# Kernel optimization log

Hardware: AMD Instinct MI355X
Metric: run time of the kernel (lower is better)

## Reference

```python
import jax, jax.numpy as jnp
import numpy as np

N_NODES = 20000
N_EDGES = 320000
IN_DIM = 256
OUT_DIM = 256
NUM_RELS = 8
NUM_BASES = 4


def setup_inputs() -> dict:
    key = jax.random.key(0)
    k = jax.random.split(key, 7)
    return {
        "h": jax.random.normal(k[0], (N_NODES, IN_DIM), dtype=jnp.float32),
        "basis": jax.random.normal(k[1], (NUM_BASES, IN_DIM, OUT_DIM), dtype=jnp.float32)
        * (6.0 / (IN_DIM + OUT_DIM)) ** 0.5,
        "w_comp": jax.random.normal(k[2], (NUM_RELS, NUM_BASES), dtype=jnp.float32),
        "bias": jax.random.normal(k[3], (OUT_DIM,), dtype=jnp.float32) * 0.01,
        "src": jax.random.randint(k[4], (N_EDGES,), 0, N_NODES, dtype=jnp.int32),
        "dst": jax.random.randint(k[5], (N_EDGES,), 0, N_NODES, dtype=jnp.int32),
        "etype": jax.random.randint(k[6], (N_EDGES,), 0, NUM_RELS, dtype=jnp.int32),
    }


def reference(h, basis, w_comp, bias, src, dst, etype):
    # Faithful to the torch basis-decomposition quirk:
    #   weight.view(in, B, out); matmul(w_comp, .) -> [in, R, out]; view -> [R, in, out]
    in_dim, out_dim = h.shape[1], basis.shape[2]
    num_rels = w_comp.shape[0]
    wr = basis.reshape(in_dim, NUM_BASES, out_dim)          # raw-buffer reinterpret (torch .view)
    weight = jnp.einsum("rb,ibo->iro", w_comp, wr)          # [in, R, out]
    weight = weight.reshape(num_rels, in_dim, out_dim)      # raw-buffer reinterpret (torch .view)

    # msg_e = h[src_e] @ weight[etype_e]. Group by relation: transform all nodes
    # under every relation weight (dense GEMMs), then gather per edge.
    t = jnp.einsum("nd,rdo->rno", h, weight)                # [R, N, out]
    msg = t[etype, src]                                     # [E, out]

    # scatter-sum aggregation to destination nodes (dgl fn.sum)
    agg = jax.ops.segment_sum(msg, dst, num_segments=h.shape[0])  # [N, out]
    return jax.nn.relu(agg + bias)
```

## Files before the change

kernel.cpp:

```cpp
#include <hip/hip_runtime.h>


#define N_NODES  20000
#define N_EDGES  320000
#define IN_DIM   256
#define OUT_DIM  256
#define NUM_RELS 8
#define KDIM     128
#define M_PAD    20032
#define CAP      96

#define FOLD_BLOCKS 2500
#define FILL_BLOCKS 1250
#define BP_BLOCKS   128

typedef __attribute__((ext_vector_type(8)))  short short8;
typedef __attribute__((ext_vector_type(16))) float float16v;

static __device__ __forceinline__ unsigned f2bf_rne(float x) {
    unsigned u = __float_as_uint(x);
    return (u + 0x7fffu + ((u >> 16) & 1u)) >> 16;
}
static __device__ __forceinline__ float bf2f(unsigned b) {
    return __uint_as_float(b << 16);
}

__global__ __launch_bounds__(256)
void prep_kernel(const float* __restrict__ h, const float* __restrict__ w_comp,
                 unsigned short* __restrict__ U,
                 const int* __restrict__ src, const int* __restrict__ dst,
                 const int* __restrict__ et,
                 int* __restrict__ cnt, int* __restrict__ bucket,
                 const float* __restrict__ basis, unsigned short* __restrict__ Bp) {
    int b = blockIdx.x;
    int t = threadIdx.x;
    if (b < FOLD_BLOCKS) {
        int gid = b * 256 + t;
        int n = gid >> 5, k = gid & 31;
        const float* hp = h + (size_t)n * IN_DIM + k * 8;
        float4 h0 = *(const float4*)hp;
        float4 h1 = *(const float4*)(hp + 4);
        float hv[8] = {h0.x, h0.y, h0.z, h0.w, h1.x, h1.y, h1.z, h1.w};
        float a0 = 0.f, a1 = 0.f, a2 = 0.f, a3 = 0.f;
#pragma unroll
        for (int j = 0; j < 8; ++j) {
            float hj = hv[j];
            a0 += hj * w_comp[j * 4 + 0];
            a1 += hj * w_comp[j * 4 + 1];
            a2 += hj * w_comp[j * 4 + 2];
            a3 += hj * w_comp[j * 4 + 3];
        }
        uint2 p;
        p.x = f2bf_rne(a0) | (f2bf_rne(a1) << 16);
        p.y = f2bf_rne(a2) | (f2bf_rne(a3) << 16);
        *(uint2*)(U + ((size_t)n << 7) + k * 4) = p;
    } else if (b < FOLD_BLOCKS + FILL_BLOCKS) {
        int e = (b - FOLD_BLOCKS) * 256 + t;
        int d = dst[e];
        int p = atomicAdd(&cnt[d], 1);
        if (p < CAP) bucket[(size_t)d * CAP + p] = src[e] | (et[e] << 16);
    } else {
        int frag = (b - FOLD_BLOCKS - FILL_BLOCKS) * 256 + t;
        int lane = frag & 63;
        int ks   = (frag >> 6) & 7;
        int r    = (frag >> 9) & 7;
        int ct   = frag >> 12;
        int o  = ct * 32 + (lane & 31);
        int kb = r * 128 + ks * 16 + (lane >> 5) * 8;
        const float* bsp = basis + (size_t)kb * 256 + o;
        unsigned v[8];
#pragma unroll
        for (int j = 0; j < 8; ++j) v[j] = f2bf_rne(bsp[(size_t)j * 256]);
        uint4 p;
        p.x = v[0] | (v[1] << 16);
        p.y = v[2] | (v[3] << 16);
        p.z = v[4] | (v[5] << 16);
        p.w = v[6] | (v[7] << 16);
        *(uint4*)(Bp + (size_t)frag * 8) = p;
    }
}

__global__ __launch_bounds__(256)
void aggregate_kernel(const unsigned short* __restrict__ U,
                      const int* __restrict__ cnt,
                      const int* __restrict__ bucket,
                      unsigned int* __restrict__ S) {
    int wid  = threadIdx.x >> 6;
    int lane = threadIdx.x & 63;
    int d = blockIdx.x * 4 + wid;
    float2 acc[NUM_RELS];
#pragma unroll
    for (int r = 0; r < NUM_RELS; ++r) { acc[r].x = 0.f; acc[r].y = 0.f; }

    if (d < N_NODES) {
        int n = cnt[d];
        if (n > CAP) n = CAP;
        const int4* bp4 = (const int4*)(bucket + (size_t)d * CAP);
        int4 ea = bp4[0], eb = bp4[1];
        for (int i = 0; i < n; i += 8) {
            int4 c0 = ea, c1 = eb;
            ea = bp4[(i >> 2) + 2];
            eb = bp4[(i >> 2) + 3];
            int m = n - i;
            int es[8] = {c0.x, c0.y, c0.z, c0.w, c1.x, c1.y, c1.z, c1.w};
            unsigned uv[8];
#pragma unroll
            for (int j = 0; j < 8; ++j) {
                int s = es[j] & 0xffff;
                uv[j] = *(const unsigned*)(U + ((size_t)s << 7) + lane * 2);
            }
#pragma unroll
            for (int j = 0; j < 8; ++j) {
                if (j < m) {
                    int r = __builtin_amdgcn_readfirstlane(es[j] >> 16);
                    float fx = bf2f(uv[j] & 0xffffu), fy = bf2f(uv[j] >> 16);
                    switch (r) {
                        case 0: acc[0].x += fx; acc[0].y += fy; break;
                        case 1: acc[1].x += fx; acc[1].y += fy; break;
                        case 2: acc[2].x += fx; acc[2].y += fy; break;
                        case 3: acc[3].x += fx; acc[3].y += fy; break;
                        case 4: acc[4].x += fx; acc[4].y += fy; break;
                        case 5: acc[5].x += fx; acc[5].y += fy; break;
                        case 6: acc[6].x += fx; acc[6].y += fy; break;
                        default: acc[7].x += fx; acc[7].y += fy; break;
                    }
                }
            }
        }
    }
#pragma unroll
    for (int r = 0; r < NUM_RELS; ++r) {
        unsigned p = f2bf_rne(acc[r].x) | (f2bf_rne(acc[r].y) << 16);
        S[(((size_t)r * M_PAD + d) << 6) + lane] = p;
    }
}

__global__ __launch_bounds__(512)
void gemm_kernel(const unsigned short* __restrict__ S,
                 const unsigned short* __restrict__ Bp,
                 const float* __restrict__ bias,
                 float* __restrict__ out) {
    __shared__ unsigned short At[32][136];
    int t = threadIdx.x;
    int w = t >> 6, lane = t & 63;
    int ln = lane & 31, hi = lane >> 5;
    int n0 = blockIdx.x * 32;
    int c0 = w * 32;

    int srow = t >> 4, sq = t & 15;
    const unsigned short* sbase = S + (((size_t)n0 + srow) << 7) + sq * 8;
    uint4 pre = *(const uint4*)sbase;

    float16v acc = {};

    for (int r = 0; r < NUM_RELS; ++r) {
        if (r > 0) __syncthreads();
        *(uint4*)&At[srow][sq * 8] = pre;
        __syncthreads();
        if (r + 1 < NUM_RELS)
            pre = *(const uint4*)(sbase + (((size_t)(r + 1) * M_PAD) << 7));
        const unsigned short* bpr = Bp + (((size_t)(w * 8 + r) * 8) << 9) + lane * 8;
#pragma unroll
        for (int ks = 0; ks < 8; ++ks) {
            short8 a  = *(const short8*)&At[ln][ks * 16 + hi * 8];
            short8 bo = *(const short8*)(bpr + (ks << 9));
            acc = __builtin_amdgcn_mfma_f32_32x32x16_bf16(a, bo, acc, 0, 0, 0);
        }
    }

    float bs = bias[c0 + ln];
#pragma unroll
    for (int reg = 0; reg < 16; ++reg) {
        int row = (reg & 3) + 8 * (reg >> 2) + 4 * hi;
        int n = n0 + row;
        if (n < N_NODES)
            out[(size_t)n * OUT_DIM + c0 + ln] = fmaxf(acc[reg] + bs, 0.f);
    }
}

extern "C" void kernel_launch(void* const* d_in, const int* in_sizes, int n_in,
                              void* d_out, int out_size, void* d_ws, size_t ws_size,
                              hipStream_t stream) {
    const float* h      = (const float*)d_in[0];
    const float* basis  = (const float*)d_in[1];
    const float* w_comp = (const float*)d_in[2];
    const float* bias   = (const float*)d_in[3];
    const int*   src    = (const int*)d_in[4];
    const int*   dst    = (const int*)d_in[5];
    const int*   etype  = (const int*)d_in[6];
    float*       out    = (float*)d_out;

    char* ws = (char*)d_ws;
    size_t off = 0;
    unsigned short* U   = (unsigned short*)(ws + off); off += (size_t)N_NODES * KDIM * 2;
    unsigned int*   S   = (unsigned int*)(ws + off);   off += (size_t)NUM_RELS * M_PAD * KDIM * 2;
    unsigned short* Bp  = (unsigned short*)(ws + off); off += (size_t)8 * 8 * 8 * 64 * 8 * 2;
    int* cnt    = (int*)(ws + off); off += (size_t)M_PAD * 4;
    int* bucket = (int*)(ws + off); off += ((size_t)M_PAD * CAP + 32) * 4;

    hipMemsetAsync(cnt, 0, (size_t)N_NODES * 4, stream);

    prep_kernel<<<FOLD_BLOCKS + FILL_BLOCKS + BP_BLOCKS, 256, 0, stream>>>(
        h, w_comp, U, src, dst, etype, cnt, bucket, basis, Bp);

    aggregate_kernel<<<M_PAD / 4, 256, 0, stream>>>(U, cnt, bucket, S);

    gemm_kernel<<<M_PAD / 32, 512, 0, stream>>>((const unsigned short*)S, Bp, bias, out);
}
```

Measured before the change: 149.1 us.

## Bucket edges per (dst, relation) and gather two edges per wavefront

Edge bucketing now keys on destination and relation together, with a 32-slot sub-bucket per pair, so the aggregation kernel no longer branches on the relation for each edge. Each wavefront splits into two halves that gather different source rows with 8-byte loads. The first edge of every relation is prefetched unconditionally, and the two halves are combined with a cross-half shuffle before the bf16 store. The cost is a larger count array and memset, more bucket memory, and reads from empty sub-buckets, which hold stale or uninitialized indices and are masked out only after the load.

```diff
diff --git a/kernel.cpp b/kernel.cpp
--- a/kernel.cpp
+++ b/kernel.cpp
@@ -8,7 +8,7 @@
 #define NUM_RELS 8
 #define KDIM     128
 #define M_PAD    20032
-#define CAP      96
+#define SUBCAP   32
 
 #define FOLD_BLOCKS 2500
 #define FILL_BLOCKS 1250
@@ -20,9 +20,6 @@
 static __device__ __forceinline__ unsigned f2bf_rne(float x) {
     unsigned u = __float_as_uint(x);
     return (u + 0x7fffu + ((u >> 16) & 1u)) >> 16;
-}
-static __device__ __forceinline__ float bf2f(unsigned b) {
-    return __uint_as_float(b << 16);
 }
 
 __global__ __launch_bounds__(256)
@@ -30,7 +27,7 @@
                  unsigned short* __restrict__ U,
                  const int* __restrict__ src, const int* __restrict__ dst,
                  const int* __restrict__ et,
-                 int* __restrict__ cnt, int* __restrict__ bucket,
+                 int* __restrict__ cnt2, int* __restrict__ bucket2,
                  const float* __restrict__ basis, unsigned short* __restrict__ Bp) {
     int b = blockIdx.x;
     int t = threadIdx.x;
@@ -56,9 +53,9 @@
         *(uint2*)(U + ((size_t)n << 7) + k * 4) = p;
     } else if (b < FOLD_BLOCKS + FILL_BLOCKS) {
         int e = (b - FOLD_BLOCKS) * 256 + t;
-        int d = dst[e];
-        int p = atomicAdd(&cnt[d], 1);
-        if (p < CAP) bucket[(size_t)d * CAP + p] = src[e] | (et[e] << 16);
+        int g = dst[e] * 8 + et[e];
+        int p = atomicAdd(&cnt2[g], 1);
+        if (p < SUBCAP) bucket2[(g << 5) + p] = src[e];
     } else {
         int frag = (b - FOLD_BLOCKS - FILL_BLOCKS) * 256 + t;
         int lane = frag & 63;
@@ -82,56 +79,71 @@
 
 __global__ __launch_bounds__(256)
 void aggregate_kernel(const unsigned short* __restrict__ U,
-                      const int* __restrict__ cnt,
-                      const int* __restrict__ bucket,
+                      const int* __restrict__ cnt2,
+                      const int* __restrict__ bucket2,
                       unsigned int* __restrict__ S) {
     int wid  = threadIdx.x >> 6;
     int lane = threadIdx.x & 63;
+    int half = lane >> 5;
+    int l32  = lane & 31;
     int d = blockIdx.x * 4 + wid;
-    float2 acc[NUM_RELS];
-#pragma unroll
-    for (int r = 0; r < NUM_RELS; ++r) { acc[r].x = 0.f; acc[r].y = 0.f; }
+
+    float4 acc[NUM_RELS];
+#pragma unroll
+    for (int r = 0; r < NUM_RELS; ++r) acc[r] = make_float4(0.f, 0.f, 0.f, 0.f);
 
     if (d < N_NODES) {
-        int n = cnt[d];
-        if (n > CAP) n = CAP;
-        const int4* bp4 = (const int4*)(bucket + (size_t)d * CAP);
-        int4 ea = bp4[0], eb = bp4[1];
-        for (int i = 0; i < n; i += 8) {
-            int4 c0 = ea, c1 = eb;
-            ea = bp4[(i >> 2) + 2];
-            eb = bp4[(i >> 2) + 3];
-            int m = n - i;
-            int es[8] = {c0.x, c0.y, c0.z, c0.w, c1.x, c1.y, c1.z, c1.w};
-            unsigned uv[8];
-#pragma unroll
-            for (int j = 0; j < 8; ++j) {
-                int s = es[j] & 0xffff;
-                uv[j] = *(const unsigned*)(U + ((size_t)s << 7) + lane * 2);
+        int base = d * 8;
+        int4 ca = *(const int4*)(cnt2 + base);
+        int4 cb = *(const int4*)(cnt2 + base + 4);
+        int c[8] = {ca.x, ca.y, ca.z, ca.w, cb.x, cb.y, cb.z, cb.w};
+#pragma unroll
+        for (int r = 0; r < 8; ++r) if (c[r] > SUBCAP) c[r] = SUBCAP;
+
+        uint2 ga[8];
+#pragma unroll
+        for (int r = 0; r < 8; ++r) {
+            int s = bucket2[((base + r) << 5) + half] & 0x7fff;
+            ga[r] = *(const uint2*)(U + ((size_t)s << 7) + l32 * 4);
+        }
+#pragma unroll
+        for (int r = 0; r < 8; ++r) {
+            if (half < c[r]) {
+                acc[r].x += __uint_as_float(ga[r].x << 16);
+                acc[r].y += __uint_as_float(ga[r].x & 0xffff0000u);
+                acc[r].z += __uint_as_float(ga[r].y << 16);
+                acc[r].w += __uint_as_float(ga[r].y & 0xffff0000u);
             }
-#pragma unroll
-            for (int j = 0; j < 8; ++j) {
-                if (j < m) {
-                    int r = __builtin_amdgcn_readfirstlane(es[j] >> 16);
-                    float fx = bf2f(uv[j] & 0xffffu), fy = bf2f(uv[j] >> 16);
-                    switch (r) {
-                        case 0: acc[0].x += fx; acc[0].y += fy; break;
-                        case 1: acc[1].x += fx; acc[1].y += fy; break;
-                        case 2: acc[2].x += fx; acc[2].y += fy; break;
-                        case 3: acc[3].x += fx; acc[3].y += fy; break;
-                        case 4: acc[4].x += fx; acc[4].y += fy; break;
-                        case 5: acc[5].x += fx; acc[5].y += fy; break;
-                        case 6: acc[6].x += fx; acc[6].y += fy; break;
-                        default: acc[7].x += fx; acc[7].y += fy; break;
-                    }
+        }
+#pragma unroll
+        for (int r = 0; r < 8; ++r) {
+            for (int i = 2; i < c[r]; i += 2) {
+                int s = bucket2[((base + r) << 5) + i + half] & 0x7fff;
+                uint2 g = *(const uint2*)(U + ((size_t)s << 7) + l32 * 4);
+                if (i + half < c[r]) {
+                    acc[r].x += __uint_as_float(g.x << 16);
+                    acc[r].y += __uint_as_float(g.x & 0xffff0000u);
+                    acc[r].z += __uint_as_float(g.y << 16);
+                    acc[r].w += __uint_as_float(g.y & 0xffff0000u);
                 }
             }
         }
     }
 #pragma unroll
     for (int r = 0; r < NUM_RELS; ++r) {
-        unsigned p = f2bf_rne(acc[r].x) | (f2bf_rne(acc[r].y) << 16);
-        S[(((size_t)r * M_PAD + d) << 6) + lane] = p;
+        acc[r].x += __shfl_xor(acc[r].x, 32);
+        acc[r].y += __shfl_xor(acc[r].y, 32);
+        acc[r].z += __shfl_xor(acc[r].z, 32);
+        acc[r].w += __shfl_xor(acc[r].w, 32);
+    }
+    if (half == 0) {
+#pragma unroll
+        for (int r = 0; r < NUM_RELS; ++r) {
+            uint2 p;
+            p.x = f2bf_rne(acc[r].x) | (f2bf_rne(acc[r].y) << 16);
+            p.y = f2bf_rne(acc[r].z) | (f2bf_rne(acc[r].w) << 16);
+            *(uint2*)(S + (((size_t)r * M_PAD + d) << 6) + l32 * 2) = p;
+        }
     }
 }
 
@@ -195,15 +207,15 @@
     unsigned short* U   = (unsigned short*)(ws + off); off += (size_t)N_NODES * KDIM * 2;
     unsigned int*   S   = (unsigned int*)(ws + off);   off += (size_t)NUM_RELS * M_PAD * KDIM * 2;
     unsigned short* Bp  = (unsigned short*)(ws + off); off += (size_t)8 * 8 * 8 * 64 * 8 * 2;
-    int* cnt    = (int*)(ws + off); off += (size_t)M_PAD * 4;
-    int* bucket = (int*)(ws + off); off += ((size_t)M_PAD * CAP + 32) * 4;
-
-    hipMemsetAsync(cnt, 0, (size_t)N_NODES * 4, stream);
+    int* cnt2    = (int*)(ws + off); off += (size_t)M_PAD * 8 * 4;
+    int* bucket2 = (int*)(ws + off); off += ((size_t)M_PAD * 8 * SUBCAP + 64) * 4;
+
+    hipMemsetAsync(cnt2, 0, (size_t)N_NODES * 8 * 4, stream);
 
     prep_kernel<<<FOLD_BLOCKS + FILL_BLOCKS + BP_BLOCKS, 256, 0, stream>>>(
-        h, w_comp, U, src, dst, etype, cnt, bucket, basis, Bp);
-
-    aggregate_kernel<<<M_PAD / 4, 256, 0, stream>>>(U, cnt, bucket, S);
+        h, w_comp, U, src, dst, etype, cnt2, bucket2, basis, Bp);
+
+    aggregate_kernel<<<M_PAD / 4, 256, 0, stream>>>(U, cnt2, bucket2, S);
 
     gemm_kernel<<<M_PAD / 32, 512, 0, stream>>>((const unsigned short*)S, Bp, bias, out);
 }
```

Result: faster. 143.4 us (-3.8%).
